# Performance work log

Measured on AMD Instinct MI355X. Metric: run time of the kernel, lower is better.

Reference implementation:

```python
import jax, jax.numpy as jnp
import numpy as np

N = 50000
E = 800000
D_IN, D_HID, D_OUT = 128, 128, 64


def gcn_layer(x, src, dst, W, b, n_nodes):
    # GCNConv: h = W x; add self-loops; symmetric normalization deg^-1/2;
    # scatter-add messages from src to dst; add bias.
    h = x @ W  # [N, d_out]
    loop = jnp.arange(n_nodes, dtype=src.dtype)
    src_sl = jnp.concatenate([src, loop])  # [E+N]
    dst_sl = jnp.concatenate([dst, loop])
    deg = jax.ops.segment_sum(jnp.ones_like(dst_sl, dtype=h.dtype), dst_sl,
                              num_segments=n_nodes)  # in-degree incl. self-loop
    dis = jnp.where(deg > 0, jax.lax.rsqrt(deg), 0.0)
    norm = dis[src_sl] * dis[dst_sl]  # [E+N]
    msg = h[src_sl] * norm[:, None]  # gather + scale
    out = jax.ops.segment_sum(msg, dst_sl, num_segments=n_nodes)
    return out + b


def setup_inputs() -> dict:
    key = jax.random.key(0)
    ks = jax.random.split(key, 8)
    x = jax.random.normal(ks[0], (N, D_IN), dtype=jnp.float32)
    edge_index = jax.random.randint(ks[1], (2, E), 0, N, dtype=jnp.int32)
    def glorot(k, fan_in, fan_out):
        s = jnp.sqrt(6.0 / (fan_in + fan_out))
        return jax.random.uniform(k, (fan_in, fan_out), jnp.float32, -s, s)
    return {
        "x": x,
        "edge_index": edge_index,
        "W1": glorot(ks[2], D_IN, D_HID),  "b1": jnp.zeros((D_HID,), jnp.float32),
        "W2": glorot(ks[3], D_HID, D_HID), "b2": jnp.zeros((D_HID,), jnp.float32),
        "W3": glorot(ks[4], D_HID, D_OUT), "b3": jnp.zeros((D_OUT,), jnp.float32),
    }


def reference(x, edge_index, W1, b1, W2, b2, W3, b3):
    src, dst = edge_index[0], edge_index[1]
    n = x.shape[0]
    h = jax.nn.relu(gcn_layer(x, src, dst, W1, b1, n))
    h = jax.nn.relu(gcn_layer(h, src, dst, W2, b2, n))
    return gcn_layer(h, src, dst, W3, b3, n)
```

## Files before the change

kernel.cpp:

```cpp
#include <hip/hip_runtime.h>
#include <hip/hip_fp16.h>
#include <math.h>


typedef _Float16 half8 __attribute__((ext_vector_type(8)));
typedef float f32x4 __attribute__((ext_vector_type(4)));

__global__ void count_kernel(const int* __restrict__ dst, int* __restrict__ counts,
                             int* __restrict__ rank, int E) {
    int i = blockIdx.x * blockDim.x + threadIdx.x;
    int st = gridDim.x * blockDim.x;
    for (; i < E; i += st) rank[i] = atomicAdd(&counts[dst[i]], 1);
}

__global__ __launch_bounds__(256) void block_sum_kernel(const int* __restrict__ counts,
                                                        int* __restrict__ bsum, int n) {
    const int b = blockIdx.x;
    const int t = threadIdx.x;
    const int idx = b * 256 + t;
    int v = (idx < n) ? counts[idx] : 0;
#pragma unroll
    for (int o = 32; o > 0; o >>= 1) v += __shfl_down(v, o, 64);
    __shared__ int ws[4];
    if ((t & 63) == 0) ws[t >> 6] = v;
    __syncthreads();
    if (t == 0) bsum[b] = ws[0] + ws[1] + ws[2] + ws[3];
}

__global__ __launch_bounds__(256) void small_scan_kernel(int* __restrict__ bsum, int nb) {
    __shared__ int sm[256];
    const int t = threadIdx.x;
    int v = (t < nb) ? bsum[t] : 0;
    sm[t] = v;
    __syncthreads();
    for (int o = 1; o < 256; o <<= 1) {
        int x = (t >= o) ? sm[t - o] : 0;
        __syncthreads();
        sm[t] += x;
        __syncthreads();
    }
    if (t < nb) bsum[t] = sm[t] - v;
}

__global__ __launch_bounds__(256) void scan_block_kernel(const int* __restrict__ counts,
                                                         const int* __restrict__ bsum,
                                                         int* __restrict__ offs,
                                                         float* __restrict__ dis,
                                                         int n, int E) {
    const int b = blockIdx.x;
    const int t = threadIdx.x;
    const int idx = b * 256 + t;
    int v = (idx < n) ? counts[idx] : 0;
    if (idx < n) dis[idx] = rsqrtf((float)(v + 1));
    __shared__ int sm[256];
    sm[t] = v;
    __syncthreads();
    for (int o = 1; o < 256; o <<= 1) {
        int x = (t >= o) ? sm[t - o] : 0;
        __syncthreads();
        sm[t] += x;
        __syncthreads();
    }
    if (idx < n) offs[idx] = bsum[b] + sm[t] - v;
    if (idx == n) offs[n] = E;
}

__global__ void fill_kernel(const int* __restrict__ src, const int* __restrict__ dst,
                            const int* __restrict__ offs, const int* __restrict__ rank,
                            int* __restrict__ csr_s, int E) {
    int i = blockIdx.x * blockDim.x + threadIdx.x;
    int st = gridDim.x * blockDim.x;
    for (; i < E; i += st) {
        int p = offs[dst[i]] + rank[i];
        csr_s[p] = src[i];
    }
}

__global__ void xsplit_kernel(const float* __restrict__ in, _Float16* __restrict__ hi,
                              _Float16* __restrict__ lo, int n8) {
    int i = blockIdx.x * blockDim.x + threadIdx.x;
    int st = gridDim.x * blockDim.x;
    const float4* in4 = (const float4*)in;
    for (; i < n8; i += st) {
        float4 v0 = in4[(size_t)i * 2];
        float4 v1 = in4[(size_t)i * 2 + 1];
        float v[8] = {v0.x, v0.y, v0.z, v0.w, v1.x, v1.y, v1.z, v1.w};
        half8 h, l;
#pragma unroll
        for (int j = 0; j < 8; ++j) {
            _Float16 hh = (_Float16)v[j];
            h[j] = hh;
            l[j] = (_Float16)(v[j] - (float)hh);
        }
        ((half8*)hi)[i] = h;
        ((half8*)lo)[i] = l;
    }
}

__global__ __launch_bounds__(256) void wsplit_kernel(const float* __restrict__ W1,
                                                     const float* __restrict__ W2,
                                                     const float* __restrict__ W3,
                                                     _Float16* __restrict__ hi,
                                                     _Float16* __restrict__ lo) {
    int idx = blockIdx.x * 256 + threadIdx.x;
    if (idx >= 40960) return;
    float v;
    if (idx < 16384) {
        int c = idx >> 7, k = idx & 127;
        v = W1[k * 128 + c];
    } else if (idx < 32768) {
        int j = idx - 16384;
        int c = j >> 7, k = j & 127;
        v = W2[k * 128 + c];
    } else {
        int j = idx - 32768;
        int c = j >> 7, k = j & 127;
        v = W3[k * 64 + c];
    }
    _Float16 h = (_Float16)v;
    hi[idx] = h;
    lo[idx] = (_Float16)(v - (float)h);
}

template <int NOUT>
__global__ __launch_bounds__(256) void gemm_mfma(const _Float16* __restrict__ Xhi,
                                                 const _Float16* __restrict__ Xlo,
                                                 const _Float16* __restrict__ WThi,
                                                 const _Float16* __restrict__ WTlo,
                                                 const float* __restrict__ dis,
                                                 _Float16* __restrict__ Y, int nrows) {
    constexpr int CT = NOUT / 16;
    const int wave = threadIdx.x >> 6;
    const int lane = threadIdx.x & 63;
    const int lrow = lane & 15;
    const int lk = lane >> 4;
    const int r0 = (blockIdx.x * 4 + wave) * 32;

    const f32x4 Z = {0.f, 0.f, 0.f, 0.f};
    f32x4 acc[2][CT];
#pragma unroll
    for (int a = 0; a < 2; ++a)
#pragma unroll
        for (int b = 0; b < CT; ++b) acc[a][b] = Z;

    const half8* XhiV = (const half8*)Xhi;
    const half8* XloV = (const half8*)Xlo;
    const half8* WhiV = (const half8*)WThi;
    const half8* WloV = (const half8*)WTlo;

    int ar0 = r0 + lrow;
    int ar1 = r0 + 16 + lrow;
    if (ar0 > nrows - 1) ar0 = nrows - 1;
    if (ar1 > nrows - 1) ar1 = nrows - 1;

#pragma unroll
    for (int ks = 0; ks < 4; ++ks) {
        const int kidx = ks * 4 + lk;
        half8 a0h = XhiV[(size_t)ar0 * 16 + kidx];
        half8 a0l = XloV[(size_t)ar0 * 16 + kidx];
        half8 a1h = XhiV[(size_t)ar1 * 16 + kidx];
        half8 a1l = XloV[(size_t)ar1 * 16 + kidx];
#pragma unroll
        for (int ct = 0; ct < CT; ++ct) {
            const size_t bidx = (size_t)(ct * 16 + lrow) * 16 + kidx;
            half8 bh = WhiV[bidx];
            half8 bl = WloV[bidx];
            acc[0][ct] = __builtin_amdgcn_mfma_f32_16x16x32_f16(a0l, bh, acc[0][ct], 0, 0, 0);
            acc[0][ct] = __builtin_amdgcn_mfma_f32_16x16x32_f16(a0h, bl, acc[0][ct], 0, 0, 0);
            acc[0][ct] = __builtin_amdgcn_mfma_f32_16x16x32_f16(a0h, bh, acc[0][ct], 0, 0, 0);
            acc[1][ct] = __builtin_amdgcn_mfma_f32_16x16x32_f16(a1l, bh, acc[1][ct], 0, 0, 0);
            acc[1][ct] = __builtin_amdgcn_mfma_f32_16x16x32_f16(a1h, bl, acc[1][ct], 0, 0, 0);
            acc[1][ct] = __builtin_amdgcn_mfma_f32_16x16x32_f16(a1h, bh, acc[1][ct], 0, 0, 0);
        }
    }

    const int orow = r0 + lk * 4;
#pragma unroll
    for (int rt = 0; rt < 2; ++rt) {
#pragma unroll
        for (int r = 0; r < 4; ++r) {
            int row = orow + rt * 16 + r;
            if (row < nrows) {
                float dd = dis[row];
#pragma unroll
                for (int ct = 0; ct < CT; ++ct) {
                    Y[(size_t)row * NOUT + ct * 16 + lrow] =
                        (_Float16)(dd * acc[rt][ct][r]);
                }
            }
        }
    }
}

template <int F, bool RELU, bool SPLIT>
__global__ __launch_bounds__(256) void agg_kernel(const __half* __restrict__ h,
                                                  const float* __restrict__ dis,
                                                  const int* __restrict__ offs,
                                                  const int* __restrict__ csr_s,
                                                  const float* __restrict__ bias,
                                                  float* __restrict__ outf,
                                                  __half* __restrict__ ohi,
                                                  __half* __restrict__ olo, int n) {
    const int d = blockIdx.x * 4 + (threadIdx.x >> 6);
    if (d >= n) return;
    const int lane = threadIdx.x & 63;
    const int beg = offs[d];
    const int end = offs[d + 1];

    float sx = 0.f, sy = 0.f;
    int i = beg;
    if constexpr (F == 128) {
        const unsigned* h32 = (const unsigned*)h;
        for (; i + 8 <= end; i += 8) {
            int s[8];
#pragma unroll
            for (int j = 0; j < 8; ++j) s[j] = csr_s[i + j];
            unsigned v[8];
#pragma unroll
            for (int j = 0; j < 8; ++j) v[j] = h32[(size_t)s[j] * 64 + lane];
#pragma unroll
            for (int j = 0; j < 8; ++j) {
                float2 vf = __half22float2(*reinterpret_cast<__half2*>(&v[j]));
                sx += vf.x;
                sy += vf.y;
            }
        }
        if (i + 4 <= end) {
            int s[4];
#pragma unroll
            for (int j = 0; j < 4; ++j) s[j] = csr_s[i + j];
            unsigned v[4];
#pragma unroll
            for (int j = 0; j < 4; ++j) v[j] = h32[(size_t)s[j] * 64 + lane];
#pragma unroll
            for (int j = 0; j < 4; ++j) {
                float2 vf = __half22float2(*reinterpret_cast<__half2*>(&v[j]));
                sx += vf.x;
                sy += vf.y;
            }
            i += 4;
        }
        for (; i < end; ++i) {
            unsigned v = h32[(size_t)csr_s[i] * 64 + lane];
            float2 vf = __half22float2(*reinterpret_cast<__half2*>(&v));
            sx += vf.x;
            sy += vf.y;
        }
        {
            unsigned v = h32[(size_t)d * 64 + lane];
            float2 vf = __half22float2(*reinterpret_cast<__half2*>(&v));
            sx += vf.x;
            sy += vf.y;
        }
        float dd = dis[d];
        float2 b2 = ((const float2*)bias)[lane];
        float rx = fmaf(dd, sx, b2.x);
        float ry = fmaf(dd, sy, b2.y);
        if (RELU) {
            rx = fmaxf(rx, 0.f);
            ry = fmaxf(ry, 0.f);
        }
        if constexpr (SPLIT) {
            __half hx = __float2half(rx), hy = __float2half(ry);
            __half lx = __float2half(rx - __half2float(hx));
            __half ly = __float2half(ry - __half2float(hy));
            ((__half2*)(ohi + (size_t)d * F))[lane] = __halves2half2(hx, hy);
            ((__half2*)(olo + (size_t)d * F))[lane] = __halves2half2(lx, ly);
        } else {
            ((float2*)(outf + (size_t)d * F))[lane] = make_float2(rx, ry);
        }
    } else {
        const unsigned short* h16 = (const unsigned short*)h;
        for (; i + 8 <= end; i += 8) {
            int s[8];
#pragma unroll
            for (int j = 0; j < 8; ++j) s[j] = csr_s[i + j];
            unsigned short v[8];
#pragma unroll
            for (int j = 0; j < 8; ++j) v[j] = h16[(size_t)s[j] * 64 + lane];
#pragma unroll
            for (int j = 0; j < 8; ++j)
                sx += __half2float(*reinterpret_cast<__half*>(&v[j]));
        }
        if (i + 4 <= end) {
            int s[4];
#pragma unroll
            for (int j = 0; j < 4; ++j) s[j] = csr_s[i + j];
            unsigned short v[4];
#pragma unroll
            for (int j = 0; j < 4; ++j) v[j] = h16[(size_t)s[j] * 64 + lane];
#pragma unroll
            for (int j = 0; j < 4; ++j)
                sx += __half2float(*reinterpret_cast<__half*>(&v[j]));
            i += 4;
        }
        for (; i < end; ++i) {
            unsigned short v = h16[(size_t)csr_s[i] * 64 + lane];
            sx += __half2float(*reinterpret_cast<__half*>(&v));
        }
        {
            unsigned short v = h16[(size_t)d * 64 + lane];
            sx += __half2float(*reinterpret_cast<__half*>(&v));
        }
        float dd = dis[d];
        float r = fmaf(dd, sx, bias[lane]);
        if (RELU) r = fmaxf(r, 0.f);
        out_store:
        if constexpr (SPLIT) {
            __half hx = __float2half(r);
            ohi[(size_t)d * F + lane] = hx;
            olo[(size_t)d * F + lane] = __float2half(r - __half2float(hx));
        } else {
            outf[(size_t)d * F + lane] = r;
        }
    }
}


extern "C" void kernel_launch(void* const* d_in, const int* in_sizes, int n_in,
                              void* d_out, int out_size, void* d_ws, size_t ws_size,
                              hipStream_t stream) {
    const float* x  = (const float*)d_in[0];
    const int*   ei = (const int*)d_in[1];
    const float* W1 = (const float*)d_in[2];
    const float* b1 = (const float*)d_in[3];
    const float* W2 = (const float*)d_in[4];
    const float* b2 = (const float*)d_in[5];
    const float* W3 = (const float*)d_in[6];
    const float* b3 = (const float*)d_in[7];

    const int N = in_sizes[0] / 128;
    const int E = in_sizes[1] / 2;
    const int* src = ei;
    const int* dst = ei + E;
    float* out = (float*)d_out;

    char* w = (char*)d_ws;
    auto take = [&](size_t bytes) -> void* {
        void* p = (void*)w;
        w += (bytes + 255) & ~(size_t)255;
        return p;
    };
    int*      counts = (int*)take((size_t)N * 4);
    int*      offs   = (int*)take((size_t)(N + 1) * 4);
    float*    dis    = (float*)take((size_t)N * 4);
    int*      bsum   = (int*)take((size_t)1024 * 4);
    int*      csr_s  = (int*)take((size_t)E * 4);
    _Float16* G16    = (_Float16*)take((size_t)N * 128 * 2);
    _Float16* Xhi    = (_Float16*)take((size_t)N * 128 * 2);
    _Float16* Xlo    = (_Float16*)take((size_t)N * 128 * 2);
    _Float16* Whi    = (_Float16*)take((size_t)40960 * 2);
    _Float16* Wlo    = (_Float16*)take((size_t)40960 * 2);
    int*      rank   = (int*)G16;

    const int NBLK = (N + 256) / 256;

    hipMemsetAsync(counts, 0, (size_t)N * 4, stream);
    count_kernel<<<2048, 256, 0, stream>>>(dst, counts, rank, E);
    block_sum_kernel<<<NBLK, 256, 0, stream>>>(counts, bsum, N);
    small_scan_kernel<<<1, 256, 0, stream>>>(bsum, NBLK);
    scan_block_kernel<<<NBLK, 256, 0, stream>>>(counts, bsum, offs, dis, N, E);
    fill_kernel<<<2048, 256, 0, stream>>>(src, dst, offs, rank, csr_s, E);

    wsplit_kernel<<<160, 256, 0, stream>>>(W1, W2, W3, Whi, Wlo);
    xsplit_kernel<<<2048, 256, 0, stream>>>(x, Xhi, Xlo, N * 16);

    const int gblocks = (N + 127) / 128;
    const int ablocks = (N + 3) / 4;

    gemm_mfma<128><<<gblocks, 256, 0, stream>>>(Xhi, Xlo, Whi, Wlo, dis, G16, N);
    agg_kernel<128, true, true><<<ablocks, 256, 0, stream>>>(
        (const __half*)G16, dis, offs, csr_s, b1, nullptr, (__half*)Xhi, (__half*)Xlo, N);
    gemm_mfma<128><<<gblocks, 256, 0, stream>>>(Xhi, Xlo, Whi + 16384, Wlo + 16384,
                                                dis, G16, N);
    agg_kernel<128, true, true><<<ablocks, 256, 0, stream>>>(
        (const __half*)G16, dis, offs, csr_s, b2, nullptr, (__half*)Xhi, (__half*)Xlo, N);
    gemm_mfma<64><<<gblocks, 256, 0, stream>>>(Xhi, Xlo, Whi + 32768, Wlo + 32768,
                                               dis, G16, N);
    agg_kernel<64, false, false><<<ablocks, 256, 0, stream>>>(
        (const __half*)G16, dis, offs, csr_s, b3, out, nullptr, nullptr, N);
}
```

Baseline: 235.5 us.

## Fuse input split into first GEMM, pair-split edges across half-waves in aggregation

The separate fp32-to-hi/lo split pass over x is removed, and the first GEMM now reads fp32 x directly and splits it in registers. The aggregation kernel now has each half-wave gather a different neighbor row with wider per-lane loads, and the two halves are combined with a cross-half shuffle. CSR fill uses an atomic cursor instead of a stored rank array. These cut the extra memory pass and make the gather issue more in parallel. The costs are an extra memcpy, atomics during fill, and edge ordering within a row that is no longer deterministic.

```diff
diff --git a/kernel.cpp b/kernel.cpp
--- a/kernel.cpp
+++ b/kernel.cpp
@@ -6,11 +6,10 @@
 typedef _Float16 half8 __attribute__((ext_vector_type(8)));
 typedef float f32x4 __attribute__((ext_vector_type(4)));
 
-__global__ void count_kernel(const int* __restrict__ dst, int* __restrict__ counts,
-                             int* __restrict__ rank, int E) {
+__global__ void count_kernel(const int* __restrict__ dst, int* __restrict__ counts, int E) {
     int i = blockIdx.x * blockDim.x + threadIdx.x;
     int st = gridDim.x * blockDim.x;
-    for (; i < E; i += st) rank[i] = atomicAdd(&counts[dst[i]], 1);
+    for (; i < E; i += st) atomicAdd(&counts[dst[i]], 1);
 }
 
 __global__ __launch_bounds__(256) void block_sum_kernel(const int* __restrict__ counts,
@@ -66,34 +65,12 @@
 }
 
 __global__ void fill_kernel(const int* __restrict__ src, const int* __restrict__ dst,
-                            const int* __restrict__ offs, const int* __restrict__ rank,
-                            int* __restrict__ csr_s, int E) {
+                            int* __restrict__ cursor, int* __restrict__ csr_s, int E) {
     int i = blockIdx.x * blockDim.x + threadIdx.x;
     int st = gridDim.x * blockDim.x;
     for (; i < E; i += st) {
-        int p = offs[dst[i]] + rank[i];
+        int p = atomicAdd(&cursor[dst[i]], 1);
         csr_s[p] = src[i];
-    }
-}
-
-__global__ void xsplit_kernel(const float* __restrict__ in, _Float16* __restrict__ hi,
-                              _Float16* __restrict__ lo, int n8) {
-    int i = blockIdx.x * blockDim.x + threadIdx.x;
-    int st = gridDim.x * blockDim.x;
-    const float4* in4 = (const float4*)in;
-    for (; i < n8; i += st) {
-        float4 v0 = in4[(size_t)i * 2];
-        float4 v1 = in4[(size_t)i * 2 + 1];
-        float v[8] = {v0.x, v0.y, v0.z, v0.w, v1.x, v1.y, v1.z, v1.w};
-        half8 h, l;
-#pragma unroll
-        for (int j = 0; j < 8; ++j) {
-            _Float16 hh = (_Float16)v[j];
-            h[j] = hh;
-            l[j] = (_Float16)(v[j] - (float)hh);
-        }
-        ((half8*)hi)[i] = h;
-        ((half8*)lo)[i] = l;
     }
 }
 
@@ -123,12 +100,13 @@
 }
 
 template <int NOUT>
-__global__ __launch_bounds__(256) void gemm_mfma(const _Float16* __restrict__ Xhi,
-                                                 const _Float16* __restrict__ Xlo,
-                                                 const _Float16* __restrict__ WThi,
-                                                 const _Float16* __restrict__ WTlo,
-                                                 const float* __restrict__ dis,
-                                                 _Float16* __restrict__ Y, int nrows) {
+__device__ __forceinline__ void gemm_core(const half8* __restrict__ XhiV,
+                                          const half8* __restrict__ XloV,
+                                          const _Float16* __restrict__ WThi,
+                                          const _Float16* __restrict__ WTlo,
+                                          const float* __restrict__ dis,
+                                          _Float16* __restrict__ Y, int nrows,
+                                          bool from_f32, const float4* X4) {
     constexpr int CT = NOUT / 16;
     const int wave = threadIdx.x >> 6;
     const int lane = threadIdx.x & 63;
@@ -143,8 +121,6 @@
 #pragma unroll
         for (int b = 0; b < CT; ++b) acc[a][b] = Z;
 
-    const half8* XhiV = (const half8*)Xhi;
-    const half8* XloV = (const half8*)Xlo;
     const half8* WhiV = (const half8*)WThi;
     const half8* WloV = (const half8*)WTlo;
 
@@ -156,10 +132,29 @@
 #pragma unroll
     for (int ks = 0; ks < 4; ++ks) {
         const int kidx = ks * 4 + lk;
-        half8 a0h = XhiV[(size_t)ar0 * 16 + kidx];
-        half8 a0l = XloV[(size_t)ar0 * 16 + kidx];
-        half8 a1h = XhiV[(size_t)ar1 * 16 + kidx];
-        half8 a1l = XloV[(size_t)ar1 * 16 + kidx];
+        half8 a0h, a0l, a1h, a1l;
+        if (from_f32) {
+            float4 u0 = X4[(size_t)ar0 * 32 + 2 * kidx];
+            float4 u1 = X4[(size_t)ar0 * 32 + 2 * kidx + 1];
+            float4 w0 = X4[(size_t)ar1 * 32 + 2 * kidx];
+            float4 w1 = X4[(size_t)ar1 * 32 + 2 * kidx + 1];
+            float v0[8] = {u0.x, u0.y, u0.z, u0.w, u1.x, u1.y, u1.z, u1.w};
+            float v1[8] = {w0.x, w0.y, w0.z, w0.w, w1.x, w1.y, w1.z, w1.w};
+#pragma unroll
+            for (int j = 0; j < 8; ++j) {
+                _Float16 hh = (_Float16)v0[j];
+                a0h[j] = hh;
+                a0l[j] = (_Float16)(v0[j] - (float)hh);
+                _Float16 gg = (_Float16)v1[j];
+                a1h[j] = gg;
+                a1l[j] = (_Float16)(v1[j] - (float)gg);
+            }
+        } else {
+            a0h = XhiV[(size_t)ar0 * 16 + kidx];
+            a0l = XloV[(size_t)ar0 * 16 + kidx];
+            a1h = XhiV[(size_t)ar1 * 16 + kidx];
+            a1l = XloV[(size_t)ar1 * 16 + kidx];
+        }
 #pragma unroll
         for (int ct = 0; ct < CT; ++ct) {
             const size_t bidx = (size_t)(ct * 16 + lrow) * 16 + kidx;
@@ -190,6 +185,26 @@
             }
         }
     }
+}
+
+template <int NOUT>
+__global__ __launch_bounds__(256) void gemm_mfma(const _Float16* __restrict__ Xhi,
+                                                 const _Float16* __restrict__ Xlo,
+                                                 const _Float16* __restrict__ WThi,
+                                                 const _Float16* __restrict__ WTlo,
+                                                 const float* __restrict__ dis,
+                                                 _Float16* __restrict__ Y, int nrows) {
+    gemm_core<NOUT>((const half8*)Xhi, (const half8*)Xlo, WThi, WTlo, dis, Y, nrows,
+                    false, nullptr);
+}
+
+__global__ __launch_bounds__(256) void gemm_mfma_l1(const float* __restrict__ X,
+                                                    const _Float16* __restrict__ WThi,
+                                                    const _Float16* __restrict__ WTlo,
+                                                    const float* __restrict__ dis,
+                                                    _Float16* __restrict__ Y, int nrows) {
+    gemm_core<128>(nullptr, nullptr, WThi, WTlo, dis, Y, nrows, true,
+                   (const float4*)X);
 }
 
 template <int F, bool RELU, bool SPLIT>
@@ -204,114 +219,176 @@
     const int d = blockIdx.x * 4 + (threadIdx.x >> 6);
     if (d >= n) return;
     const int lane = threadIdx.x & 63;
+    const int li = lane & 31;
+    const bool upper = lane >= 32;
     const int beg = offs[d];
     const int end = offs[d + 1];
 
-    float sx = 0.f, sy = 0.f;
-    int i = beg;
     if constexpr (F == 128) {
-        const unsigned* h32 = (const unsigned*)h;
-        for (; i + 8 <= end; i += 8) {
+        const uint2* hv = (const uint2*)h;
+        float a0 = 0.f, a1 = 0.f, a2 = 0.f, a3 = 0.f;
+        int i = beg;
+        for (; i + 16 <= end; i += 16) {
+            int s[16];
+#pragma unroll
+            for (int j = 0; j < 16; ++j) s[j] = csr_s[i + j];
+            uint2 v[8];
+#pragma unroll
+            for (int p = 0; p < 8; ++p) {
+                int row = upper ? s[2 * p + 1] : s[2 * p];
+                v[p] = hv[(size_t)row * 32 + li];
+            }
+#pragma unroll
+            for (int p = 0; p < 8; ++p) {
+                float2 f0 = __half22float2(*reinterpret_cast<__half2*>(&v[p].x));
+                float2 f1 = __half22float2(*reinterpret_cast<__half2*>(&v[p].y));
+                a0 += f0.x; a1 += f0.y; a2 += f1.x; a3 += f1.y;
+            }
+        }
+        if (i + 8 <= end) {
             int s[8];
 #pragma unroll
             for (int j = 0; j < 8; ++j) s[j] = csr_s[i + j];
+            uint2 v[4];
+#pragma unroll
+            for (int p = 0; p < 4; ++p) {
+                int row = upper ? s[2 * p + 1] : s[2 * p];
+                v[p] = hv[(size_t)row * 32 + li];
+            }
+#pragma unroll
+            for (int p = 0; p < 4; ++p) {
+                float2 f0 = __half22float2(*reinterpret_cast<__half2*>(&v[p].x));
+                float2 f1 = __half22float2(*reinterpret_cast<__half2*>(&v[p].y));
+                a0 += f0.x; a1 += f0.y; a2 += f1.x; a3 += f1.y;
+            }
+            i += 8;
+        }
+        for (; i + 2 <= end; i += 2) {
+            int s0 = csr_s[i], s1 = csr_s[i + 1];
+            int row = upper ? s1 : s0;
+            uint2 v = hv[(size_t)row * 32 + li];
+            float2 f0 = __half22float2(*reinterpret_cast<__half2*>(&v.x));
+            float2 f1 = __half22float2(*reinterpret_cast<__half2*>(&v.y));
+            a0 += f0.x; a1 += f0.y; a2 += f1.x; a3 += f1.y;
+        }
+        if (!upper) {
+            if (i < end) {
+                uint2 v = hv[(size_t)csr_s[i] * 32 + li];
+                float2 f0 = __half22float2(*reinterpret_cast<__half2*>(&v.x));
+                float2 f1 = __half22float2(*reinterpret_cast<__half2*>(&v.y));
+                a0 += f0.x; a1 += f0.y; a2 += f1.x; a3 += f1.y;
+            }
+            {
+                uint2 v = hv[(size_t)d * 32 + li];
+                float2 f0 = __half22float2(*reinterpret_cast<__half2*>(&v.x));
+                float2 f1 = __half22float2(*reinterpret_cast<__half2*>(&v.y));
+                a0 += f0.x; a1 += f0.y; a2 += f1.x; a3 += f1.y;
+            }
+        }
+        a0 += __shfl_xor(a0, 32);
+        a1 += __shfl_xor(a1, 32);
+        a2 += __shfl_xor(a2, 32);
+        a3 += __shfl_xor(a3, 32);
+        if (!upper) {
+            float dd = dis[d];
+            float4 b4 = ((const float4*)bias)[li];
+            float r0 = fmaf(dd, a0, b4.x);
+            float r1 = fmaf(dd, a1, b4.y);
+            float r2 = fmaf(dd, a2, b4.z);
+            float r3 = fmaf(dd, a3, b4.w);
+            if (RELU) {
+                r0 = fmaxf(r0, 0.f); r1 = fmaxf(r1, 0.f);
+                r2 = fmaxf(r2, 0.f); r3 = fmaxf(r3, 0.f);
+            }
+            if constexpr (SPLIT) {
+                __half h0 = __float2half(r0), h1 = __float2half(r1);
+                __half h2 = __float2half(r2), h3 = __float2half(r3);
+                __half2 hh01 = __halves2half2(h0, h1), hh23 = __halves2half2(h2, h3);
+                uint2 uh;
+                uh.x = *reinterpret_cast<unsigned*>(&hh01);
+                uh.y = *reinterpret_cast<unsigned*>(&hh23);
+                ((uint2*)ohi)[(size_t)d * 32 + li] = uh;
+                __half l0 = __float2half(r0 - __half2float(h0));
+                __half l1 = __float2half(r1 - __half2float(h1));
+                __half l2 = __float2half(r2 - __half2float(h2));
+                __half l3 = __float2half(r3 - __half2float(h3));
+                __half2 ll01 = __halves2half2(l0, l1), ll23 = __halves2half2(l2, l3);
+                uint2 ul;
+                ul.x = *reinterpret_cast<unsigned*>(&ll01);
+                ul.y = *reinterpret_cast<unsigned*>(&ll23);
+                ((uint2*)olo)[(size_t)d * 32 + li] = ul;
+            } else {
+                ((float4*)outf)[(size_t)d * 32 + li] = make_float4(r0, r1, r2, r3);
+            }
+        }
+    } else {
+        const unsigned* hv = (const unsigned*)h;
+        float a0 = 0.f, a1 = 0.f;
+        int i = beg;
+        for (; i + 16 <= end; i += 16) {
+            int s[16];
+#pragma unroll
+            for (int j = 0; j < 16; ++j) s[j] = csr_s[i + j];
             unsigned v[8];
 #pragma unroll
-            for (int j = 0; j < 8; ++j) v[j] = h32[(size_t)s[j] * 64 + lane];
-#pragma unroll
-            for (int j = 0; j < 8; ++j) {
-                float2 vf = __half22float2(*reinterpret_cast<__half2*>(&v[j]));
-                sx += vf.x;
-                sy += vf.y;
-            }
-        }
-        if (i + 4 <= end) {
-            int s[4];
-#pragma unroll
-            for (int j = 0; j < 4; ++j) s[j] = csr_s[i + j];
+            for (int p = 0; p < 8; ++p) {
+                int row = upper ? s[2 * p + 1] : s[2 * p];
+                v[p] = hv[(size_t)row * 32 + li];
+            }
+#pragma unroll
+            for (int p = 0; p < 8; ++p) {
+                float2 f = __half22float2(*reinterpret_cast<__half2*>(&v[p]));
+                a0 += f.x; a1 += f.y;
+            }
+        }
+        if (i + 8 <= end) {
+            int s[8];
+#pragma unroll
+            for (int j = 0; j < 8; ++j) s[j] = csr_s[i + j];
             unsigned v[4];
 #pragma unroll
-            for (int j = 0; j < 4; ++j) v[j] = h32[(size_t)s[j] * 64 + lane];
-#pragma unroll
-            for (int j = 0; j < 4; ++j) {
-                float2 vf = __half22float2(*reinterpret_cast<__half2*>(&v[j]));
-                sx += vf.x;
-                sy += vf.y;
-            }
-            i += 4;
-        }
-        for (; i < end; ++i) {
-            unsigned v = h32[(size_t)csr_s[i] * 64 + lane];
-            float2 vf = __half22float2(*reinterpret_cast<__half2*>(&v));
-            sx += vf.x;
-            sy += vf.y;
-        }
-        {
-            unsigned v = h32[(size_t)d * 64 + lane];
-            float2 vf = __half22float2(*reinterpret_cast<__half2*>(&v));
-            sx += vf.x;
-            sy += vf.y;
-        }
-        float dd = dis[d];
-        float2 b2 = ((const float2*)bias)[lane];
-        float rx = fmaf(dd, sx, b2.x);
-        float ry = fmaf(dd, sy, b2.y);
-        if (RELU) {
-            rx = fmaxf(rx, 0.f);
-            ry = fmaxf(ry, 0.f);
-        }
-        if constexpr (SPLIT) {
-            __half hx = __float2half(rx), hy = __float2half(ry);
-            __half lx = __float2half(rx - __half2float(hx));
-            __half ly = __float2half(ry - __half2float(hy));
-            ((__half2*)(ohi + (size_t)d * F))[lane] = __halves2half2(hx, hy);
-            ((__half2*)(olo + (size_t)d * F))[lane] = __halves2half2(lx, ly);
-        } else {
-            ((float2*)(outf + (size_t)d * F))[lane] = make_float2(rx, ry);
-        }
-    } else {
-        const unsigned short* h16 = (const unsigned short*)h;
-        for (; i + 8 <= end; i += 8) {
-            int s[8];
-#pragma unroll
-            for (int j = 0; j < 8; ++j) s[j] = csr_s[i + j];
-            unsigned short v[8];
-#pragma unroll
-            for (int j = 0; j < 8; ++j) v[j] = h16[(size_t)s[j] * 64 + lane];
-#pragma unroll
-            for (int j = 0; j < 8; ++j)
-                sx += __half2float(*reinterpret_cast<__half*>(&v[j]));
-        }
-        if (i + 4 <= end) {
-            int s[4];
-#pragma unroll
-            for (int j = 0; j < 4; ++j) s[j] = csr_s[i + j];
-            unsigned short v[4];
-#pragma unroll
-            for (int j = 0; j < 4; ++j) v[j] = h16[(size_t)s[j] * 64 + lane];
-#pragma unroll
-            for (int j = 0; j < 4; ++j)
-                sx += __half2float(*reinterpret_cast<__half*>(&v[j]));
-            i += 4;
-        }
-        for (; i < end; ++i) {
-            unsigned short v = h16[(size_t)csr_s[i] * 64 + lane];
-            sx += __half2float(*reinterpret_cast<__half*>(&v));
-        }
-        {
-            unsigned short v = h16[(size_t)d * 64 + lane];
-            sx += __half2float(*reinterpret_cast<__half*>(&v));
-        }
-        float dd = dis[d];
-        float r = fmaf(dd, sx, bias[lane]);
-        if (RELU) r = fmaxf(r, 0.f);
-        out_store:
-        if constexpr (SPLIT) {
-            __half hx = __float2half(r);
-            ohi[(size_t)d * F + lane] = hx;
-            olo[(size_t)d * F + lane] = __float2half(r - __half2float(hx));
-        } else {
-            outf[(size_t)d * F + lane] = r;
+            for (int p = 0; p < 4; ++p) {
+                int row = upper ? s[2 * p + 1] : s[2 * p];
+                v[p] = hv[(size_t)row * 32 + li];
+            }
+#pragma unroll
+            for (int p = 0; p < 4; ++p) {
+                float2 f = __half22float2(*reinterpret_cast<__half2*>(&v[p]));
+                a0 += f.x; a1 += f.y;
+            }
+            i += 8;
+        }
+        for (; i + 2 <= end; i += 2) {
+            int s0 = csr_s[i], s1 = csr_s[i + 1];
+            int row = upper ? s1 : s0;
+            unsigned v = hv[(size_t)row * 32 + li];
+            float2 f = __half22float2(*reinterpret_cast<__half2*>(&v));
+            a0 += f.x; a1 += f.y;
+        }
+        if (!upper) {
+            if (i < end) {
+                unsigned v = hv[(size_t)csr_s[i] * 32 + li];
+                float2 f = __half22float2(*reinterpret_cast<__half2*>(&v));
+                a0 += f.x; a1 += f.y;
+            }
+            {
+                unsigned v = hv[(size_t)d * 32 + li];
+                float2 f = __half22float2(*reinterpret_cast<__half2*>(&v));
+                a0 += f.x; a1 += f.y;
+            }
+        }
+        a0 += __shfl_xor(a0, 32);
+        a1 += __shfl_xor(a1, 32);
+        if (!upper) {
+            float dd = dis[d];
+            float2 b2 = ((const float2*)bias)[li];
+            float r0 = fmaf(dd, a0, b2.x);
+            float r1 = fmaf(dd, a1, b2.y);
+            if (RELU) {
+                r0 = fmaxf(r0, 0.f);
+                r1 = fmaxf(r1, 0.f);
+            }
+            ((float2*)outf)[(size_t)d * 32 + li] = make_float2(r0, r1);
         }
     }
 }
@@ -343,6 +420,7 @@
     };
     int*      counts = (int*)take((size_t)N * 4);
     int*      offs   = (int*)take((size_t)(N + 1) * 4);
+    int*      cursor = (int*)take((size_t)N * 4);
     float*    dis    = (float*)take((size_t)N * 4);
     int*      bsum   = (int*)take((size_t)1024 * 4);
     int*      csr_s  = (int*)take((size_t)E * 4);
@@ -351,24 +429,23 @@
     _Float16* Xlo    = (_Float16*)take((size_t)N * 128 * 2);
     _Float16* Whi    = (_Float16*)take((size_t)40960 * 2);
     _Float16* Wlo    = (_Float16*)take((size_t)40960 * 2);
-    int*      rank   = (int*)G16;
 
     const int NBLK = (N + 256) / 256;
 
     hipMemsetAsync(counts, 0, (size_t)N * 4, stream);
-    count_kernel<<<2048, 256, 0, stream>>>(dst, counts, rank, E);
+    count_kernel<<<2048, 256, 0, stream>>>(dst, counts, E);
     block_sum_kernel<<<NBLK, 256, 0, stream>>>(counts, bsum, N);
     small_scan_kernel<<<1, 256, 0, stream>>>(bsum, NBLK);
     scan_block_kernel<<<NBLK, 256, 0, stream>>>(counts, bsum, offs, dis, N, E);
-    fill_kernel<<<2048, 256, 0, stream>>>(src, dst, offs, rank, csr_s, E);
+    hipMemcpyAsync(cursor, offs, (size_t)N * 4, hipMemcpyDeviceToDevice, stream);
+    fill_kernel<<<2048, 256, 0, stream>>>(src, dst, cursor, csr_s, E);
 
     wsplit_kernel<<<160, 256, 0, stream>>>(W1, W2, W3, Whi, Wlo);
-    xsplit_kernel<<<2048, 256, 0, stream>>>(x, Xhi, Xlo, N * 16);
 
     const int gblocks = (N + 127) / 128;
     const int ablocks = (N + 3) / 4;
 
-    gemm_mfma<128><<<gblocks, 256, 0, stream>>>(Xhi, Xlo, Whi, Wlo, dis, G16, N);
+    gemm_mfma_l1<<<gblocks, 256, 0, stream>>>(x, Whi, Wlo, dis, G16, N);
     agg_kernel<128, true, true><<<ablocks, 256, 0, stream>>>(
         (const __half*)G16, dis, offs, csr_s, b1, nullptr, (__half*)Xhi, (__half*)Xlo, N);
     gemm_mfma<128><<<gblocks, 256, 0, stream>>>(Xhi, Xlo, Whi + 16384, Wlo + 16384,
```

Measured after the change: 336.9 us. +43.1%, slower.
